# Kernel optimization log

Measured on AMD Instinct MI355X. Metric: run time of the kernel, lower is better.

Reference implementation:

```python
import jax, jax.numpy as jnp
import numpy as np

N = 20000        # nodes
E = 320000       # edges (avg degree 16)
F_IN = 256       # n_feat
HID = 64         # n_hid (per-head channels, layer 1)
HEADS = 8        # hard-coded n_head in GAT2
NCLS = 64        # n_classes
NEG_SLOPE = 0.2  # PyG GATv2Conv default leaky_relu slope
EPS = 1e-16      # PyG softmax denominator epsilon


def setup_inputs() -> dict:
    key = jax.random.key(0)
    ks = jax.random.split(key, 10)
    glorot = lambda k, shape: jax.random.normal(k, shape, jnp.float32) * (1.0 / np.sqrt(shape[0]))
    return {
        "x": jax.random.normal(ks[0], (N, F_IN), jnp.float32),
        "edge_index": jax.random.randint(ks[1], (2, E), 0, N, dtype=jnp.int32),
        # layer 1: GATv2Conv(F_IN -> HID, heads=HEADS, concat=True)
        "Wl1": glorot(ks[2], (F_IN, HEADS * HID)),
        "Wr1": glorot(ks[3], (F_IN, HEADS * HID)),
        "att1": glorot(ks[4], (HEADS, HID)),
        "b1": jnp.zeros((HEADS * HID,), jnp.float32),
        # layer 2: GATv2Conv(HEADS*HID -> NCLS, heads=1, concat=False)
        "Wl2": glorot(ks[5], (HEADS * HID, NCLS)),
        "Wr2": glorot(ks[6], (HEADS * HID, NCLS)),
        "att2": glorot(ks[7], (1, NCLS)),
        "b2": jnp.zeros((NCLS,), jnp.float32),
    }


def gatv2_layer(x, Wl, Wr, att, bias, src, dst, heads, concat):
    # x: [N, Fin]; Wl/Wr: [Fin, heads*C]; att: [heads, C]
    n = x.shape[0]
    c = att.shape[1]
    xl = (x @ Wl).reshape(n, heads, c)   # source-side projection
    xr = (x @ Wr).reshape(n, heads, c)   # target-side projection
    # per-edge GATv2 score: a^T leaky_relu(Wl x_j + Wr x_i)
    e = jax.nn.leaky_relu(xl[src] + xr[dst], NEG_SLOPE)      # [E, H, C]
    alpha = jnp.einsum('ehc,hc->eh', e, att)                 # [E, H]
    # segment softmax over incoming edges of each target node
    amax = jax.ops.segment_max(alpha, dst, num_segments=n)   # [N, H]
    amax = jnp.where(jnp.isfinite(amax), amax, 0.0)
    ex = jnp.exp(alpha - amax[dst])
    denom = jax.ops.segment_sum(ex, dst, num_segments=n)     # [N, H]
    w = ex / (denom[dst] + EPS)                              # [E, H]
    # weighted scatter-aggregate of source features
    out = jax.ops.segment_sum(xl[src] * w[:, :, None], dst, num_segments=n)  # [N, H, C]
    out = out.reshape(n, heads * c) if concat else out.mean(axis=1)
    return out + bias


def reference(x, edge_index, Wl1, Wr1, att1, b1, Wl2, Wr2, att2, b2):
    src, dst = edge_index[0], edge_index[1]
    h = gatv2_layer(x, Wl1, Wr1, att1, b1, src, dst, HEADS, True)   # [N, 512]
    h = jax.nn.elu(h)
    out = gatv2_layer(h, Wl2, Wr2, att2, b2, src, dst, 1, False)    # [N, 64]
    return out
```

## Files before the change

kernel.cpp:

```cpp
#include <hip/hip_runtime.h>
#include <hip/hip_bf16.h>

#define N_NODES 20000
#define N_EDGES 320000
#define F_IN 256
#define HID 64
#define HEADS 8
#define NCLS 64
#define D1 (HEADS * HID)
#define NEG_SLOPE 0.2f
#define SCAN_BLOCKS ((N_NODES + 255) / 256)

typedef __attribute__((ext_vector_type(8))) short short8;
typedef __attribute__((ext_vector_type(4))) float floatx4;

__device__ __forceinline__ ushort f2bf(float f) {
    unsigned u = __float_as_uint(f);
    unsigned r = (u + 0x7fffu + ((u >> 16) & 1u)) >> 16;
    return (ushort)r;
}
__device__ __forceinline__ float bf2f(ushort u) {
    return __uint_as_float((unsigned)u << 16);
}

__global__ __launch_bounds__(256) void convert_bf16_vec(const float* __restrict__ in,
                                                        ushort* __restrict__ out, int n4) {
    int i = blockIdx.x * 256 + threadIdx.x;
    if (i < n4) {
        float4 v = ((const float4*)in)[i];
        ushort4 o;
        o.x = f2bf(v.x); o.y = f2bf(v.y); o.z = f2bf(v.z); o.w = f2bf(v.w);
        ((ushort4*)out)[i] = o;
    }
}

__global__ __launch_bounds__(256) void transpose_w_bf16(const float* __restrict__ W,
                                                        ushort* __restrict__ Wt,
                                                        int kshift, int Nd, int total) {
    int i = blockIdx.x * 256 + threadIdx.x;
    if (i < total) {
        int n = i >> kshift, k = i & ((1 << kshift) - 1);
        Wt[i] = f2bf(W[(size_t)k * Nd + n]);
    }
}

__global__ void hist_kernel(const int* __restrict__ dst, int* __restrict__ cnt, int E) {
    int i = blockIdx.x * 256 + threadIdx.x;
    if (i < E) atomicAdd(&cnt[dst[i]], 1);
}

__global__ __launch_bounds__(256) void scan_local(const int* __restrict__ cnt,
                                                  int* __restrict__ pscan,
                                                  int* __restrict__ bsum, int n) {
    int tid = threadIdx.x;
    int i = blockIdx.x * 256 + tid;
    int lane = tid & 63, wave = tid >> 6;
    int v = (i < n) ? cnt[i] : 0;
    int x = v;
    #pragma unroll
    for (int d = 1; d < 64; d <<= 1) {
        int y = __shfl_up(x, d);
        if (lane >= d) x += y;
    }
    __shared__ int wsum[4];
    if (lane == 63) wsum[wave] = x;
    __syncthreads();
    int woff = 0;
    for (int w2 = 0; w2 < wave; w2++) woff += wsum[w2];
    int incl = x + woff;
    if (i < n) pscan[i] = incl;
    if (tid == 255) bsum[blockIdx.x] = incl;
}

__global__ __launch_bounds__(128) void scan_block(int* __restrict__ bsum, int nb) {
    int tid = threadIdx.x;
    __shared__ int sh[128];
    int v = (tid < nb) ? bsum[tid] : 0;
    sh[tid] = v;
    __syncthreads();
    #pragma unroll
    for (int d = 1; d < 128; d <<= 1) {
        int x = (tid >= d) ? sh[tid - d] : 0;
        __syncthreads();
        sh[tid] += x;
        __syncthreads();
    }
    if (tid < nb) bsum[tid] = sh[tid] - v;
}

__global__ __launch_bounds__(256) void scan_finalize(const int* __restrict__ cnt,
                                                     const int* __restrict__ pscan,
                                                     const int* __restrict__ bsum,
                                                     int* __restrict__ row_ptr,
                                                     int* __restrict__ cursor, int n) {
    int i = blockIdx.x * 256 + threadIdx.x;
    if (i < n) {
        int incl = pscan[i] + bsum[blockIdx.x];
        row_ptr[i + 1] = incl;
        cursor[i] = incl - cnt[i];
    }
    if (i == 0) row_ptr[0] = 0;
}

__global__ void scatter_kernel(const int* __restrict__ src, const int* __restrict__ dst,
                               int* __restrict__ cursor, int* __restrict__ csr_src, int E) {
    int i = blockIdx.x * 256 + threadIdx.x;
    if (i < E) {
        int d = dst[i];
        int pos = atomicAdd(&cursor[d], 1);
        csr_src[pos] = src[i];
    }
}

#define APAD 40
__global__ __launch_bounds__(256) void gemm_mfma_bt_bf16(
    const ushort* __restrict__ A, const ushort* __restrict__ Bt,
    ushort* __restrict__ C, int M, int N, int K) {
    __shared__ ushort As[128 * APAD];
    __shared__ ushort Bs[64 * APAD];
    int tid = threadIdx.x;
    int rowBase = blockIdx.y * 128, colBase = blockIdx.x * 64;
    int wave = tid >> 6, lane = tid & 63;
    int quad = lane >> 4, m16 = lane & 15;
    floatx4 acc[2][4];
    #pragma unroll
    for (int i = 0; i < 2; i++)
        #pragma unroll
        for (int j = 0; j < 4; j++) acc[i][j] = (floatx4){0.f, 0.f, 0.f, 0.f};

    for (int k0 = 0; k0 < K; k0 += 32) {
        #pragma unroll
        for (int i = 0; i < 2; i++) {
            int idx = i * 256 + tid;
            int r = idx >> 2, kq = (idx & 3) * 8;
            int grow = rowBase + r;
            uint4 v = make_uint4(0, 0, 0, 0);
            if (grow < M) v = *(const uint4*)(A + (size_t)grow * K + k0 + kq);
            *(uint4*)&As[r * APAD + kq] = v;
        }
        {
            int r = tid >> 2, kq = (tid & 3) * 8;
            uint4 v = *(const uint4*)(Bt + (size_t)(colBase + r) * K + k0 + kq);
            *(uint4*)&Bs[r * APAD + kq] = v;
        }
        __syncthreads();
        short8 a0 = *(short8*)&As[(wave * 32 + m16) * APAD + quad * 8];
        short8 a1 = *(short8*)&As[(wave * 32 + 16 + m16) * APAD + quad * 8];
        #pragma unroll
        for (int ct = 0; ct < 4; ct++) {
            short8 b = *(short8*)&Bs[(ct * 16 + m16) * APAD + quad * 8];
            acc[0][ct] = __builtin_amdgcn_mfma_f32_16x16x32_bf16(a0, b, acc[0][ct], 0, 0, 0);
            acc[1][ct] = __builtin_amdgcn_mfma_f32_16x16x32_bf16(a1, b, acc[1][ct], 0, 0, 0);
        }
        __syncthreads();
    }
    #pragma unroll
    for (int rt = 0; rt < 2; rt++)
        #pragma unroll
        for (int ct = 0; ct < 4; ct++)
            #pragma unroll
            for (int r = 0; r < 4; r++) {
                int row = rowBase + wave * 32 + rt * 16 + quad * 4 + r;
                if (row < M) C[(size_t)row * N + colBase + ct * 16 + m16] = f2bf(acc[rt][ct][r]);
            }
}

__global__ __launch_bounds__(128) void attn_l1_fused(
    const ushort* __restrict__ xlr, const float* __restrict__ att,
    const float* __restrict__ b1,
    const int* __restrict__ row_ptr, const int* __restrict__ csr_src,
    ushort* __restrict__ h1out) {
    int d = blockIdx.x, t = threadIdx.x;
    int start = row_ptr[d], deg = row_ptr[d + 1] - start;

    ushort4 xru = *(const ushort4*)(xlr + (size_t)d * 1024 + 512 + 4 * t);
    float xr0 = bf2f(xru.x), xr1 = bf2f(xru.y), xr2 = bf2f(xru.z), xr3 = bf2f(xru.w);
    float4 atv = *(const float4*)(att + 4 * t);

    float den = 0.f, acc0 = 0.f, acc1 = 0.f, acc2 = 0.f, acc3 = 0.f;

    if (deg > 0) {
        ushort4 xv[4];
        #pragma unroll
        for (int j = 0; j < 4; j++) {
            int p = min(j, deg - 1);
            int s = csr_src[start + p];
            xv[j] = *(const ushort4*)(xlr + (size_t)s * 1024 + 4 * t);
        }
        for (int p0 = 0; p0 < deg; p0 += 4) {
            ushort4 u0 = xv[0], u1 = xv[1], u2 = xv[2], u3 = xv[3];
            #pragma unroll
            for (int j = 0; j < 4; j++) {
                int p = p0 + 4 + j;
                if (p < deg) {
                    int s = csr_src[start + p];
                    xv[j] = *(const ushort4*)(xlr + (size_t)s * 1024 + 4 * t);
                }
            }
            float c00 = bf2f(u0.x), c01 = bf2f(u0.y), c02 = bf2f(u0.z), c03 = bf2f(u0.w);
            float c10 = bf2f(u1.x), c11 = bf2f(u1.y), c12 = bf2f(u1.z), c13 = bf2f(u1.w);
            float c20 = bf2f(u2.x), c21 = bf2f(u2.y), c22 = bf2f(u2.z), c23 = bf2f(u2.w);
            float c30 = bf2f(u3.x), c31 = bf2f(u3.y), c32 = bf2f(u3.z), c33 = bf2f(u3.w);
            float v;
            float p0v, p1v, p2v, p3v;
            v = c00 + xr0; v = v > 0.f ? v : NEG_SLOPE * v; p0v = atv.x * v;
            v = c01 + xr1; v = v > 0.f ? v : NEG_SLOPE * v; p0v = fmaf(atv.y, v, p0v);
            v = c02 + xr2; v = v > 0.f ? v : NEG_SLOPE * v; p0v = fmaf(atv.z, v, p0v);
            v = c03 + xr3; v = v > 0.f ? v : NEG_SLOPE * v; p0v = fmaf(atv.w, v, p0v);
            v = c10 + xr0; v = v > 0.f ? v : NEG_SLOPE * v; p1v = atv.x * v;
            v = c11 + xr1; v = v > 0.f ? v : NEG_SLOPE * v; p1v = fmaf(atv.y, v, p1v);
            v = c12 + xr2; v = v > 0.f ? v : NEG_SLOPE * v; p1v = fmaf(atv.z, v, p1v);
            v = c13 + xr3; v = v > 0.f ? v : NEG_SLOPE * v; p1v = fmaf(atv.w, v, p1v);
            v = c20 + xr0; v = v > 0.f ? v : NEG_SLOPE * v; p2v = atv.x * v;
            v = c21 + xr1; v = v > 0.f ? v : NEG_SLOPE * v; p2v = fmaf(atv.y, v, p2v);
            v = c22 + xr2; v = v > 0.f ? v : NEG_SLOPE * v; p2v = fmaf(atv.z, v, p2v);
            v = c23 + xr3; v = v > 0.f ? v : NEG_SLOPE * v; p2v = fmaf(atv.w, v, p2v);
            v = c30 + xr0; v = v > 0.f ? v : NEG_SLOPE * v; p3v = atv.x * v;
            v = c31 + xr1; v = v > 0.f ? v : NEG_SLOPE * v; p3v = fmaf(atv.y, v, p3v);
            v = c32 + xr2; v = v > 0.f ? v : NEG_SLOPE * v; p3v = fmaf(atv.z, v, p3v);
            v = c33 + xr3; v = v > 0.f ? v : NEG_SLOPE * v; p3v = fmaf(atv.w, v, p3v);
            #pragma unroll
            for (int mask = 1; mask < 16; mask <<= 1) {
                p0v += __shfl_xor(p0v, mask);
                p1v += __shfl_xor(p1v, mask);
                p2v += __shfl_xor(p2v, mask);
                p3v += __shfl_xor(p3v, mask);
            }
            float e0 = (p0 + 0 < deg) ? __expf(p0v) : 0.f;
            float e1 = (p0 + 1 < deg) ? __expf(p1v) : 0.f;
            float e2 = (p0 + 2 < deg) ? __expf(p2v) : 0.f;
            float e3 = (p0 + 3 < deg) ? __expf(p3v) : 0.f;
            den += (e0 + e1) + (e2 + e3);
            acc0 = fmaf(e0, c00, fmaf(e1, c10, fmaf(e2, c20, fmaf(e3, c30, acc0))));
            acc1 = fmaf(e0, c01, fmaf(e1, c11, fmaf(e2, c21, fmaf(e3, c31, acc1))));
            acc2 = fmaf(e0, c02, fmaf(e1, c12, fmaf(e2, c22, fmaf(e3, c32, acc2))));
            acc3 = fmaf(e0, c03, fmaf(e1, c13, fmaf(e2, c23, fmaf(e3, c33, acc3))));
        }
    }
    float inv = 1.f / (den + 1e-16f);
    float4 bv = *(const float4*)(b1 + 4 * t);
    float o0 = acc0 * inv + bv.x;
    float o1 = acc1 * inv + bv.y;
    float o2 = acc2 * inv + bv.z;
    float o3 = acc3 * inv + bv.w;
    o0 = o0 > 0.f ? o0 : (__expf(o0) - 1.f);
    o1 = o1 > 0.f ? o1 : (__expf(o1) - 1.f);
    o2 = o2 > 0.f ? o2 : (__expf(o2) - 1.f);
    o3 = o3 > 0.f ? o3 : (__expf(o3) - 1.f);
    ushort4 hv;
    hv.x = f2bf(o0); hv.y = f2bf(o1); hv.z = f2bf(o2); hv.w = f2bf(o3);
    *(ushort4*)(h1out + (size_t)d * D1 + 4 * t) = hv;
}

__global__ __launch_bounds__(256) void attn_l2_fused(
    const ushort* __restrict__ ylr, const float* __restrict__ att2,
    const float* __restrict__ b2,
    const int* __restrict__ row_ptr, const int* __restrict__ csr_src,
    float* __restrict__ out) {
    int wave = threadIdx.x >> 6, lane = threadIdx.x & 63;
    int d = blockIdx.x * 4 + wave;
    if (d >= N_NODES) return;
    int start = row_ptr[d], deg = row_ptr[d + 1] - start;

    float yrv = bf2f(ylr[(size_t)d * 128 + 64 + lane]);
    float attv = att2[lane];
    float den = 0.f, acc = 0.f;

    if (deg > 0) {
        float yv[4];
        #pragma unroll
        for (int j = 0; j < 4; j++) {
            int p = min(j, deg - 1);
            int s = csr_src[start + p];
            yv[j] = bf2f(ylr[(size_t)s * 128 + lane]);
        }
        for (int p0 = 0; p0 < deg; p0 += 4) {
            float c0 = yv[0], c1 = yv[1], c2 = yv[2], c3 = yv[3];
            #pragma unroll
            for (int j = 0; j < 4; j++) {
                int p = p0 + 4 + j;
                if (p < deg) {
                    int s = csr_src[start + p];
                    yv[j] = bf2f(ylr[(size_t)s * 128 + lane]);
                }
            }
            float v;
            v = c0 + yrv; v = v > 0.f ? v : NEG_SLOPE * v; float a0 = attv * v;
            v = c1 + yrv; v = v > 0.f ? v : NEG_SLOPE * v; float a1 = attv * v;
            v = c2 + yrv; v = v > 0.f ? v : NEG_SLOPE * v; float a2 = attv * v;
            v = c3 + yrv; v = v > 0.f ? v : NEG_SLOPE * v; float a3 = attv * v;
            #pragma unroll
            for (int mask = 1; mask < 64; mask <<= 1) {
                a0 += __shfl_xor(a0, mask);
                a1 += __shfl_xor(a1, mask);
                a2 += __shfl_xor(a2, mask);
                a3 += __shfl_xor(a3, mask);
            }
            float e0 = (p0 + 0 < deg) ? __expf(a0) : 0.f;
            float e1 = (p0 + 1 < deg) ? __expf(a1) : 0.f;
            float e2 = (p0 + 2 < deg) ? __expf(a2) : 0.f;
            float e3 = (p0 + 3 < deg) ? __expf(a3) : 0.f;
            den += (e0 + e1) + (e2 + e3);
            acc = fmaf(e0, c0, fmaf(e1, c1, fmaf(e2, c2, fmaf(e3, c3, acc))));
        }
    }
    out[(size_t)d * NCLS + lane] = acc / (den + 1e-16f) + b2[lane];
}

extern "C" void kernel_launch(void* const* d_in, const int* in_sizes, int n_in,
                              void* d_out, int out_size, void* d_ws, size_t ws_size,
                              hipStream_t stream) {
    const float* x    = (const float*)d_in[0];
    const int*   edge = (const int*)d_in[1];
    const float* Wl1  = (const float*)d_in[2];
    const float* Wr1  = (const float*)d_in[3];
    const float* att1 = (const float*)d_in[4];
    const float* b1   = (const float*)d_in[5];
    const float* Wl2  = (const float*)d_in[6];
    const float* Wr2  = (const float*)d_in[7];
    const float* att2 = (const float*)d_in[8];
    const float* b2   = (const float*)d_in[9];
    float* out = (float*)d_out;

    const int* srcv = edge;
    const int* dstv = edge + N_EDGES;

    ushort* xbf  = (ushort*)d_ws;
    ushort* wt1  = xbf + (size_t)N_NODES * F_IN;
    ushort* wt2  = wt1 + 2 * D1 * F_IN;
    ushort* xlr  = wt2 + 2 * NCLS * D1;
    ushort* h1   = xlr + (size_t)N_NODES * 2 * D1;
    ushort* ylr  = h1 + (size_t)N_NODES * D1;
    int* cnt     = (int*)(ylr + (size_t)N_NODES * 2 * NCLS);
    int* pscan   = cnt + N_NODES;
    int* bsum    = pscan + N_NODES;
    int* row_ptr = bsum + 128;
    int* cursor  = row_ptr + N_NODES + 1;
    int* csr_src = cursor + N_NODES;

    convert_bf16_vec<<<(N_NODES * F_IN / 4 + 255) / 256, 256, 0, stream>>>(x, xbf, N_NODES * F_IN / 4);
    transpose_w_bf16<<<(D1 * F_IN + 255) / 256, 256, 0, stream>>>(Wl1, wt1, 8, D1, D1 * F_IN);
    transpose_w_bf16<<<(D1 * F_IN + 255) / 256, 256, 0, stream>>>(Wr1, wt1 + D1 * F_IN, 8, D1, D1 * F_IN);
    transpose_w_bf16<<<(NCLS * D1 + 255) / 256, 256, 0, stream>>>(Wl2, wt2, 9, NCLS, NCLS * D1);
    transpose_w_bf16<<<(NCLS * D1 + 255) / 256, 256, 0, stream>>>(Wr2, wt2 + NCLS * D1, 9, NCLS, NCLS * D1);

    hipMemsetAsync(cnt, 0, N_NODES * sizeof(int), stream);
    hist_kernel<<<N_EDGES / 256, 256, 0, stream>>>(dstv, cnt, N_EDGES);
    scan_local<<<SCAN_BLOCKS, 256, 0, stream>>>(cnt, pscan, bsum, N_NODES);
    scan_block<<<1, 128, 0, stream>>>(bsum, SCAN_BLOCKS);
    scan_finalize<<<SCAN_BLOCKS, 256, 0, stream>>>(cnt, pscan, bsum, row_ptr, cursor, N_NODES);
    scatter_kernel<<<N_EDGES / 256, 256, 0, stream>>>(srcv, dstv, cursor, csr_src, N_EDGES);

    gemm_mfma_bt_bf16<<<dim3(2 * D1 / 64, (N_NODES + 127) / 128), 256, 0, stream>>>(
        xbf, wt1, xlr, N_NODES, 2 * D1, F_IN);
    attn_l1_fused<<<N_NODES, 128, 0, stream>>>(xlr, att1, b1, row_ptr, csr_src, h1);
    gemm_mfma_bt_bf16<<<dim3(2 * NCLS / 64, (N_NODES + 127) / 128), 256, 0, stream>>>(
        h1, wt2, ylr, N_NODES, 2 * NCLS, D1);
    attn_l2_fused<<<(N_NODES + 3) / 4, 256, 0, stream>>>(ylr, att2, b2, row_ptr, csr_src, out);
}
```

Measured before the change: 263.8 us.

## Merge preprocessing launches and vectorize attention kernels with packed math and DPP reductions

Folds the bf16 conversion, the four weight transposes and the degree histogram into one block-partitioned preprocess launch, cutting five launches. In both attention kernels it rewrites leaky_relu as 0.6v+0.4|v| using packed two-float vector math, and replaces the shfl_xor reductions with DPP/swizzle row sums. Layer 2 splits each wave into two halves that each handle alternate edges with two channels per lane, then combines the halves with one cross-half shuffle. This adds DPP-specific code and changes the floating-point rounding of the score computation.

```diff
diff --git a/kernel.cpp b/kernel.cpp
--- a/kernel.cpp
+++ b/kernel.cpp
@@ -8,11 +8,11 @@
 #define HEADS 8
 #define NCLS 64
 #define D1 (HEADS * HID)
-#define NEG_SLOPE 0.2f
 #define SCAN_BLOCKS ((N_NODES + 255) / 256)
 
 typedef __attribute__((ext_vector_type(8))) short short8;
 typedef __attribute__((ext_vector_type(4))) float floatx4;
+typedef __attribute__((ext_vector_type(2))) float v2f;
 
 __device__ __forceinline__ ushort f2bf(float f) {
     unsigned u = __float_as_uint(f);
@@ -22,31 +22,72 @@
 __device__ __forceinline__ float bf2f(ushort u) {
     return __uint_as_float((unsigned)u << 16);
 }
-
-__global__ __launch_bounds__(256) void convert_bf16_vec(const float* __restrict__ in,
-                                                        ushort* __restrict__ out, int n4) {
-    int i = blockIdx.x * 256 + threadIdx.x;
-    if (i < n4) {
-        float4 v = ((const float4*)in)[i];
-        ushort4 o;
-        o.x = f2bf(v.x); o.y = f2bf(v.y); o.z = f2bf(v.z); o.w = f2bf(v.w);
-        ((ushort4*)out)[i] = o;
-    }
-}
-
-__global__ __launch_bounds__(256) void transpose_w_bf16(const float* __restrict__ W,
-                                                        ushort* __restrict__ Wt,
-                                                        int kshift, int Nd, int total) {
-    int i = blockIdx.x * 256 + threadIdx.x;
-    if (i < total) {
-        int n = i >> kshift, k = i & ((1 << kshift) - 1);
-        Wt[i] = f2bf(W[(size_t)k * Nd + n]);
-    }
-}
-
-__global__ void hist_kernel(const int* __restrict__ dst, int* __restrict__ cnt, int E) {
-    int i = blockIdx.x * 256 + threadIdx.x;
-    if (i < E) atomicAdd(&cnt[dst[i]], 1);
+__device__ __forceinline__ v2f unpack2(unsigned u) {
+    v2f r;
+    r.x = __uint_as_float(u << 16);
+    r.y = __uint_as_float(u & 0xffff0000u);
+    return r;
+}
+template <int CTRL>
+__device__ __forceinline__ float dppadd(float x) {
+    int y = __builtin_amdgcn_update_dpp(0, __float_as_int(x), CTRL, 0xF, 0xF, true);
+    return x + __int_as_float(y);
+}
+__device__ __forceinline__ float rowsum16(float x) {
+    x = dppadd<0xB1>(x);
+    x = dppadd<0x4E>(x);
+    x = dppadd<0x124>(x);
+    x = dppadd<0x128>(x);
+    return x;
+}
+__device__ __forceinline__ float rowsum32(float x) {
+    x = rowsum16(x);
+    float t = __int_as_float(__builtin_amdgcn_ds_swizzle(__float_as_int(x), 0x401F));
+    return x + t;
+}
+
+#define PB_HIST 1250
+#define PB_CONV 5000
+#define PB_T1   512
+#define PB_T2   128
+#define PB_TOTAL (PB_HIST + PB_CONV + 2 * PB_T1 + 2 * PB_T2)
+__global__ __launch_bounds__(256) void preprocess(
+    const float* __restrict__ x, ushort* __restrict__ xbf,
+    const float* __restrict__ Wl1, const float* __restrict__ Wr1,
+    const float* __restrict__ Wl2, const float* __restrict__ Wr2,
+    ushort* __restrict__ wt1, ushort* __restrict__ wt2,
+    const int* __restrict__ dst, int* __restrict__ cnt) {
+    int b = blockIdx.x, t = threadIdx.x;
+    if (b < PB_HIST) {
+        int i = b * 256 + t;
+        if (i < N_EDGES) atomicAdd(&cnt[dst[i]], 1);
+    } else if (b < PB_HIST + PB_CONV) {
+        int i = (b - PB_HIST) * 256 + t;
+        if (i < N_NODES * F_IN / 4) {
+            float4 v = ((const float4*)x)[i];
+            ushort4 o;
+            o.x = f2bf(v.x); o.y = f2bf(v.y); o.z = f2bf(v.z); o.w = f2bf(v.w);
+            ((ushort4*)xbf)[i] = o;
+        }
+    } else if (b < PB_HIST + PB_CONV + 2 * PB_T1) {
+        int lb = b - PB_HIST - PB_CONV;
+        const float* W = (lb < PB_T1) ? Wl1 : Wr1;
+        ushort* Wt = wt1 + ((lb < PB_T1) ? 0 : D1 * F_IN);
+        int i = (lb % PB_T1) * 256 + t;
+        if (i < D1 * F_IN) {
+            int n = i >> 8, k = i & 255;
+            Wt[i] = f2bf(W[(size_t)k * D1 + n]);
+        }
+    } else {
+        int lb = b - PB_HIST - PB_CONV - 2 * PB_T1;
+        const float* W = (lb < PB_T2) ? Wl2 : Wr2;
+        ushort* Wt = wt2 + ((lb < PB_T2) ? 0 : NCLS * D1);
+        int i = (lb % PB_T2) * 256 + t;
+        if (i < NCLS * D1) {
+            int n = i >> 9, k = i & 511;
+            Wt[i] = f2bf(W[(size_t)k * NCLS + n]);
+        }
+    }
 }
 
 __global__ __launch_bounds__(256) void scan_local(const int* __restrict__ cnt,
@@ -173,76 +214,74 @@
     int d = blockIdx.x, t = threadIdx.x;
     int start = row_ptr[d], deg = row_ptr[d + 1] - start;
 
-    ushort4 xru = *(const ushort4*)(xlr + (size_t)d * 1024 + 512 + 4 * t);
-    float xr0 = bf2f(xru.x), xr1 = bf2f(xru.y), xr2 = bf2f(xru.z), xr3 = bf2f(xru.w);
+    uint2 xru = *(const uint2*)(xlr + (size_t)d * 1024 + 512 + 4 * t);
+    v2f xr01 = unpack2(xru.x), xr23 = unpack2(xru.y);
     float4 atv = *(const float4*)(att + 4 * t);
-
-    float den = 0.f, acc0 = 0.f, acc1 = 0.f, acc2 = 0.f, acc3 = 0.f;
+    v2f at6_01 = {0.6f * atv.x, 0.6f * atv.y}, at6_23 = {0.6f * atv.z, 0.6f * atv.w};
+    v2f at4_01 = {0.4f * atv.x, 0.4f * atv.y}, at4_23 = {0.4f * atv.z, 0.4f * atv.w};
+
+    float den = 0.f;
+    v2f acc01 = {0.f, 0.f}, acc23 = {0.f, 0.f};
 
     if (deg > 0) {
-        ushort4 xv[4];
+        uint2 xv[4];
         #pragma unroll
         for (int j = 0; j < 4; j++) {
-            int p = min(j, deg - 1);
-            int s = csr_src[start + p];
-            xv[j] = *(const ushort4*)(xlr + (size_t)s * 1024 + 4 * t);
+            int s = csr_src[start + min(j, deg - 1)];
+            xv[j] = *(const uint2*)(xlr + (size_t)s * 1024 + 4 * t);
         }
         for (int p0 = 0; p0 < deg; p0 += 4) {
-            ushort4 u0 = xv[0], u1 = xv[1], u2 = xv[2], u3 = xv[3];
+            uint2 u0 = xv[0], u1 = xv[1], u2 = xv[2], u3 = xv[3];
             #pragma unroll
             for (int j = 0; j < 4; j++) {
                 int p = p0 + 4 + j;
                 if (p < deg) {
                     int s = csr_src[start + p];
-                    xv[j] = *(const ushort4*)(xlr + (size_t)s * 1024 + 4 * t);
+                    xv[j] = *(const uint2*)(xlr + (size_t)s * 1024 + 4 * t);
                 }
             }
-            float c00 = bf2f(u0.x), c01 = bf2f(u0.y), c02 = bf2f(u0.z), c03 = bf2f(u0.w);
-            float c10 = bf2f(u1.x), c11 = bf2f(u1.y), c12 = bf2f(u1.z), c13 = bf2f(u1.w);
-            float c20 = bf2f(u2.x), c21 = bf2f(u2.y), c22 = bf2f(u2.z), c23 = bf2f(u2.w);
-            float c30 = bf2f(u3.x), c31 = bf2f(u3.y), c32 = bf2f(u3.z), c33 = bf2f(u3.w);
-            float v;
-            float p0v, p1v, p2v, p3v;
-            v = c00 + xr0; v = v > 0.f ? v : NEG_SLOPE * v; p0v = atv.x * v;
-            v = c01 + xr1; v = v > 0.f ? v : NEG_SLOPE * v; p0v = fmaf(atv.y, v, p0v);
-            v = c02 + xr2; v = v > 0.f ? v : NEG_SLOPE * v; p0v = fmaf(atv.z, v, p0v);
-            v = c03 + xr3; v = v > 0.f ? v : NEG_SLOPE * v; p0v = fmaf(atv.w, v, p0v);
-            v = c10 + xr0; v = v > 0.f ? v : NEG_SLOPE * v; p1v = atv.x * v;
-            v = c11 + xr1; v = v > 0.f ? v : NEG_SLOPE * v; p1v = fmaf(atv.y, v, p1v);
-            v = c12 + xr2; v = v > 0.f ? v : NEG_SLOPE * v; p1v = fmaf(atv.z, v, p1v);
-            v = c13 + xr3; v = v > 0.f ? v : NEG_SLOPE * v; p1v = fmaf(atv.w, v, p1v);
-            v = c20 + xr0; v = v > 0.f ? v : NEG_SLOPE * v; p2v = atv.x * v;
-            v = c21 + xr1; v = v > 0.f ? v : NEG_SLOPE * v; p2v = fmaf(atv.y, v, p2v);
-            v = c22 + xr2; v = v > 0.f ? v : NEG_SLOPE * v; p2v = fmaf(atv.z, v, p2v);
-            v = c23 + xr3; v = v > 0.f ? v : NEG_SLOPE * v; p2v = fmaf(atv.w, v, p2v);
-            v = c30 + xr0; v = v > 0.f ? v : NEG_SLOPE * v; p3v = atv.x * v;
-            v = c31 + xr1; v = v > 0.f ? v : NEG_SLOPE * v; p3v = fmaf(atv.y, v, p3v);
-            v = c32 + xr2; v = v > 0.f ? v : NEG_SLOPE * v; p3v = fmaf(atv.z, v, p3v);
-            v = c33 + xr3; v = v > 0.f ? v : NEG_SLOPE * v; p3v = fmaf(atv.w, v, p3v);
-            #pragma unroll
-            for (int mask = 1; mask < 16; mask <<= 1) {
-                p0v += __shfl_xor(p0v, mask);
-                p1v += __shfl_xor(p1v, mask);
-                p2v += __shfl_xor(p2v, mask);
-                p3v += __shfl_xor(p3v, mask);
-            }
-            float e0 = (p0 + 0 < deg) ? __expf(p0v) : 0.f;
-            float e1 = (p0 + 1 < deg) ? __expf(p1v) : 0.f;
-            float e2 = (p0 + 2 < deg) ? __expf(p2v) : 0.f;
-            float e3 = (p0 + 3 < deg) ? __expf(p3v) : 0.f;
+            v2f c01_0 = unpack2(u0.x), c23_0 = unpack2(u0.y);
+            v2f c01_1 = unpack2(u1.x), c23_1 = unpack2(u1.y);
+            v2f c01_2 = unpack2(u2.x), c23_2 = unpack2(u2.y);
+            v2f c01_3 = unpack2(u3.x), c23_3 = unpack2(u3.y);
+
+            v2f va, vb, sp;
+            va = c01_0 + xr01; vb = c23_0 + xr23;
+            sp = at6_01 * va + at4_01 * __builtin_elementwise_abs(va)
+               + at6_23 * vb + at4_23 * __builtin_elementwise_abs(vb);
+            float s0 = sp.x + sp.y;
+            va = c01_1 + xr01; vb = c23_1 + xr23;
+            sp = at6_01 * va + at4_01 * __builtin_elementwise_abs(va)
+               + at6_23 * vb + at4_23 * __builtin_elementwise_abs(vb);
+            float s1 = sp.x + sp.y;
+            va = c01_2 + xr01; vb = c23_2 + xr23;
+            sp = at6_01 * va + at4_01 * __builtin_elementwise_abs(va)
+               + at6_23 * vb + at4_23 * __builtin_elementwise_abs(vb);
+            float s2 = sp.x + sp.y;
+            va = c01_3 + xr01; vb = c23_3 + xr23;
+            sp = at6_01 * va + at4_01 * __builtin_elementwise_abs(va)
+               + at6_23 * vb + at4_23 * __builtin_elementwise_abs(vb);
+            float s3 = sp.x + sp.y;
+
+            s0 = rowsum16(s0); s1 = rowsum16(s1);
+            s2 = rowsum16(s2); s3 = rowsum16(s3);
+
+            float e0 = (p0 + 0 < deg) ? __expf(s0) : 0.f;
+            float e1 = (p0 + 1 < deg) ? __expf(s1) : 0.f;
+            float e2 = (p0 + 2 < deg) ? __expf(s2) : 0.f;
+            float e3 = (p0 + 3 < deg) ? __expf(s3) : 0.f;
             den += (e0 + e1) + (e2 + e3);
-            acc0 = fmaf(e0, c00, fmaf(e1, c10, fmaf(e2, c20, fmaf(e3, c30, acc0))));
-            acc1 = fmaf(e0, c01, fmaf(e1, c11, fmaf(e2, c21, fmaf(e3, c31, acc1))));
-            acc2 = fmaf(e0, c02, fmaf(e1, c12, fmaf(e2, c22, fmaf(e3, c32, acc2))));
-            acc3 = fmaf(e0, c03, fmaf(e1, c13, fmaf(e2, c23, fmaf(e3, c33, acc3))));
+            v2f e0v = {e0, e0}, e1v = {e1, e1}, e2v = {e2, e2}, e3v = {e3, e3};
+            acc01 = acc01 + e0v * c01_0 + e1v * c01_1 + e2v * c01_2 + e3v * c01_3;
+            acc23 = acc23 + e0v * c23_0 + e1v * c23_1 + e2v * c23_2 + e3v * c23_3;
         }
     }
     float inv = 1.f / (den + 1e-16f);
     float4 bv = *(const float4*)(b1 + 4 * t);
-    float o0 = acc0 * inv + bv.x;
-    float o1 = acc1 * inv + bv.y;
-    float o2 = acc2 * inv + bv.z;
-    float o3 = acc3 * inv + bv.w;
+    float o0 = acc01.x * inv + bv.x;
+    float o1 = acc01.y * inv + bv.y;
+    float o2 = acc23.x * inv + bv.z;
+    float o3 = acc23.y * inv + bv.w;
     o0 = o0 > 0.f ? o0 : (__expf(o0) - 1.f);
     o1 = o1 > 0.f ? o1 : (__expf(o1) - 1.f);
     o2 = o2 > 0.f ? o2 : (__expf(o2) - 1.f);
@@ -260,51 +299,57 @@
     int wave = threadIdx.x >> 6, lane = threadIdx.x & 63;
     int d = blockIdx.x * 4 + wave;
     if (d >= N_NODES) return;
+    int half = lane >> 5, l31 = lane & 31;
     int start = row_ptr[d], deg = row_ptr[d + 1] - start;
 
-    float yrv = bf2f(ylr[(size_t)d * 128 + 64 + lane]);
-    float attv = att2[lane];
-    float den = 0.f, acc = 0.f;
+    unsigned yru = *(const unsigned*)(ylr + (size_t)d * 128 + 64 + 2 * l31);
+    v2f yr2 = unpack2(yru);
+    float2 a2 = *(const float2*)(att2 + 2 * l31);
+    v2f at6 = {0.6f * a2.x, 0.6f * a2.y};
+    v2f at4 = {0.4f * a2.x, 0.4f * a2.y};
+
+    float den = 0.f;
+    v2f acc = {0.f, 0.f};
 
     if (deg > 0) {
-        float yv[4];
+        int S = (deg + 1) >> 1;
+        unsigned yv[4];
         #pragma unroll
         for (int j = 0; j < 4; j++) {
-            int p = min(j, deg - 1);
+            int p = min(2 * j + half, deg - 1);
             int s = csr_src[start + p];
-            yv[j] = bf2f(ylr[(size_t)s * 128 + lane]);
-        }
-        for (int p0 = 0; p0 < deg; p0 += 4) {
-            float c0 = yv[0], c1 = yv[1], c2 = yv[2], c3 = yv[3];
-            #pragma unroll
-            for (int j = 0; j < 4; j++) {
-                int p = p0 + 4 + j;
-                if (p < deg) {
-                    int s = csr_src[start + p];
-                    yv[j] = bf2f(ylr[(size_t)s * 128 + lane]);
-                }
+            yv[j] = *(const unsigned*)(ylr + (size_t)s * 128 + 2 * l31);
+        }
+        for (int i = 0; i < S; i++) {
+            unsigned cu = yv[i & 3];
+            int pf = i + 4;
+            if (pf < S) {
+                int p = min(2 * pf + half, deg - 1);
+                int s = csr_src[start + p];
+                yv[i & 3] = *(const unsigned*)(ylr + (size_t)s * 128 + 2 * l31);
             }
-            float v;
-            v = c0 + yrv; v = v > 0.f ? v : NEG_SLOPE * v; float a0 = attv * v;
-            v = c1 + yrv; v = v > 0.f ? v : NEG_SLOPE * v; float a1 = attv * v;
-            v = c2 + yrv; v = v > 0.f ? v : NEG_SLOPE * v; float a2 = attv * v;
-            v = c3 + yrv; v = v > 0.f ? v : NEG_SLOPE * v; float a3 = attv * v;
-            #pragma unroll
-            for (int mask = 1; mask < 64; mask <<= 1) {
-                a0 += __shfl_xor(a0, mask);
-                a1 += __shfl_xor(a1, mask);
-                a2 += __shfl_xor(a2, mask);
-                a3 += __shfl_xor(a3, mask);
-            }
-            float e0 = (p0 + 0 < deg) ? __expf(a0) : 0.f;
-            float e1 = (p0 + 1 < deg) ? __expf(a1) : 0.f;
-            float e2 = (p0 + 2 < deg) ? __expf(a2) : 0.f;
-            float e3 = (p0 + 3 < deg) ? __expf(a3) : 0.f;
-            den += (e0 + e1) + (e2 + e3);
-            acc = fmaf(e0, c0, fmaf(e1, c1, fmaf(e2, c2, fmaf(e3, c3, acc))));
-        }
-    }
-    out[(size_t)d * NCLS + lane] = acc / (den + 1e-16f) + b2[lane];
+            v2f c2 = unpack2(cu);
+            v2f v = c2 + yr2;
+            v2f sp = at6 * v + at4 * __builtin_elementwise_abs(v);
+            float sc = sp.x + sp.y;
+            sc = rowsum32(sc);
+            float e = (2 * i + half < deg) ? __expf(sc) : 0.f;
+            den += e;
+            v2f ev = {e, e};
+            acc = acc + ev * c2;
+        }
+        den += __shfl_xor(den, 32);
+        acc.x += __shfl_xor(acc.x, 32);
+        acc.y += __shfl_xor(acc.y, 32);
+    }
+    if (half == 0) {
+        float inv = 1.f / (den + 1e-16f);
+        float2 bv = *(const float2*)(b2 + 2 * l31);
+        float2 o;
+        o.x = acc.x * inv + bv.x;
+        o.y = acc.y * inv + bv.y;
+        *(float2*)(out + (size_t)d * NCLS + 2 * l31) = o;
+    }
 }
 
 extern "C" void kernel_launch(void* const* d_in, const int* in_sizes, int n_in,
@@ -338,14 +383,8 @@
     int* cursor  = row_ptr + N_NODES + 1;
     int* csr_src = cursor + N_NODES;
 
-    convert_bf16_vec<<<(N_NODES * F_IN / 4 + 255) / 256, 256, 0, stream>>>(x, xbf, N_NODES * F_IN / 4);
-    transpose_w_bf16<<<(D1 * F_IN + 255) / 256, 256, 0, stream>>>(Wl1, wt1, 8, D1, D1 * F_IN);
-    transpose_w_bf16<<<(D1 * F_IN + 255) / 256, 256, 0, stream>>>(Wr1, wt1 + D1 * F_IN, 8, D1, D1 * F_IN);
-    transpose_w_bf16<<<(NCLS * D1 + 255) / 256, 256, 0, stream>>>(Wl2, wt2, 9, NCLS, NCLS * D1);
-    transpose_w_bf16<<<(NCLS * D1 + 255) / 256, 256, 0, stream>>>(Wr2, wt2 + NCLS * D1, 9, NCLS, NCLS * D1);
-
     hipMemsetAsync(cnt, 0, N_NODES * sizeof(int), stream);
-    hist_kernel<<<N_EDGES / 256, 256, 0, stream>>>(dstv, cnt, N_EDGES);
+    preprocess<<<PB_TOTAL, 256, 0, stream>>>(x, xbf, Wl1, Wr1, Wl2, Wr2, wt1, wt2, dstv, cnt);
     scan_local<<<SCAN_BLOCKS, 256, 0, stream>>>(cnt, pscan, bsum, N_NODES);
     scan_block<<<1, 128, 0, stream>>>(bsum, SCAN_BLOCKS);
     scan_finalize<<<SCAN_BLOCKS, 256, 0, stream>>>(cnt, pscan, bsum, row_ptr, cursor, N_NODES);
```

Result: faster. 238.6 us (-9.5%).
